# Kernel tuning notes

Hardware: AMD Instinct MI355X
Metric: run time of the kernel (lower is better)

Reference implementation:

```python
import jax, jax.numpy as jnp
import numpy as np

B, S, D, H, FF = 4, 2048, 512, 8, 2048
HD = D // H
SCALE = float(D) ** 0.5  # original scales by sqrt(embed_dim), not sqrt(head_dim)
EPS = 1e-5


def setup_inputs() -> dict:
    key = jax.random.key(0)
    ks = jax.random.split(key, 16)
    s_in = 1.0 / np.sqrt(D)
    s_ff = 1.0 / np.sqrt(FF)
    return {
        "embeddings": jax.random.normal(ks[0], (B, S, D), dtype=jnp.float32),
        "mask": jnp.ones((B, S), dtype=bool),
        # per-head Q/K/V projections stacked: [H, D, HD]
        "Wq": jax.random.uniform(ks[1], (H, D, HD), jnp.float32, -s_in, s_in),
        "bq": jax.random.uniform(ks[2], (H, HD), jnp.float32, -s_in, s_in),
        "Wk": jax.random.uniform(ks[3], (H, D, HD), jnp.float32, -s_in, s_in),
        "bk": jax.random.uniform(ks[4], (H, HD), jnp.float32, -s_in, s_in),
        "Wv": jax.random.uniform(ks[5], (H, D, HD), jnp.float32, -s_in, s_in),
        "bv": jax.random.uniform(ks[6], (H, HD), jnp.float32, -s_in, s_in),
        "Wc": jax.random.uniform(ks[7], (D, D), jnp.float32, -s_in, s_in),
        "bc": jax.random.uniform(ks[8], (D,), jnp.float32, -s_in, s_in),
        "W1": jax.random.uniform(ks[9], (D, FF), jnp.float32, -s_in, s_in),
        "b1": jax.random.uniform(ks[10], (FF,), jnp.float32, -s_in, s_in),
        "W2": jax.random.uniform(ks[11], (FF, D), jnp.float32, -s_ff, s_ff),
        "b2": jax.random.uniform(ks[12], (D,), jnp.float32, -s_ff, s_ff),
        "gamma": jnp.ones((D,), jnp.float32),
        "beta": jnp.zeros((D,), jnp.float32),
    }


def reference(embeddings, mask, Wq, bq, Wk, bk, Wv, bv, Wc, bc, W1, b1, W2, b2, gamma, beta):
    # Per-head projections batched into one einsum each: [B,H,S,HD]
    Q = jnp.einsum("bsd,hdf->bhsf", embeddings, Wq) + bq[:, None, :]
    K = jnp.einsum("bsd,hdf->bhsf", embeddings, Wk) + bk[:, None, :]
    V = jnp.einsum("bsd,hdf->bhsf", embeddings, Wv) + bv[:, None, :]
    # NOTE: the original computes a masked score tensor but then softmaxes the
    # UNMASKED scores (bug). We faithfully ignore the mask here.
    scores = jnp.einsum("bhsf,bhtf->bhst", Q, K) / SCALE  # [B,H,S,S]
    A = jax.nn.softmax(scores, axis=-1)
    Hh = jnp.einsum("bhst,bhtf->bhsf", A, V)  # [B,H,S,HD]
    # concat heads along feature dim (head h -> contiguous slice)
    Hcat = jnp.transpose(Hh, (0, 2, 1, 3)).reshape(B, S, D)
    Hp = Hcat @ Wc + bc
    # add & norm (dropout is identity at eval)
    res = Hp + embeddings
    mu = jnp.mean(res, axis=-1, keepdims=True)
    var = jnp.var(res, axis=-1, keepdims=True)
    Hn = (res - mu) / jnp.sqrt(var + EPS) * gamma + beta
    out = jax.nn.relu(Hn @ W1 + b1) @ W2 + b2  # no residual after FFN in original
    return out, mask
```

## Files before the change

kernel.cpp:

```cpp
#include <hip/hip_runtime.h>
#include <hip/hip_bf16.h>
#include <cstdint>
#include <cstddef>

typedef short  s16x8 __attribute__((ext_vector_type(8)));
typedef short  s16x4 __attribute__((ext_vector_type(4)));
typedef float  f32x4 __attribute__((ext_vector_type(4)));
typedef unsigned u32x2 __attribute__((ext_vector_type(2)));

static constexpr int Bb = 4, Ss = 2048, Dd = 512, Hh = 8, HDd = 64, FFf = 2048;
static constexpr int Mm = Bb * Ss;

__device__ __forceinline__ unsigned short f2bf(float f) {
  unsigned u = __float_as_uint(f);
  u += 0x7FFFu + ((u >> 16) & 1u);
  return (unsigned short)(u >> 16);
}

__device__ __forceinline__ unsigned cvt_pk_bf16(float lo, float hi) {
  unsigned r;
  asm("v_cvt_pk_bf16_f32 %0, %1, %2" : "=v"(r) : "v"(lo), "v"(hi));
  return r;
}

#define GLOAD_LDS16(gp, lp)                                                     \
  __builtin_amdgcn_global_load_lds((const __attribute__((address_space(1))) void*)(gp), \
                                   (__attribute__((address_space(3))) void*)(lp), 16, 0, 0)

__device__ __forceinline__ void xpose_tile(const float* __restrict__ in,
                                           unsigned short* __restrict__ out,
                                           int K, int N, int bx, int by, float (*t)[33]) {
  const int lx = threadIdx.x & 31, ly = threadIdx.x >> 5;
  const int n0 = bx * 32, k0 = by * 32;
#pragma unroll
  for (int r = 0; r < 4; ++r) t[ly + r * 8][lx] = in[(size_t)(k0 + ly + r * 8) * N + n0 + lx];
  __syncthreads();
#pragma unroll
  for (int r = 0; r < 4; ++r)
    out[(size_t)(n0 + ly + r * 8) * K + k0 + lx] = f2bf(t[lx][ly + r * 8]);
}

__global__ __launch_bounds__(256) void prep_all(
    const float* __restrict__ emb, const float* __restrict__ Wq, const float* __restrict__ Wk,
    const float* __restrict__ Wv, const float* __restrict__ Wc, const float* __restrict__ W1,
    const float* __restrict__ W2, unsigned short* __restrict__ embB,
    unsigned short* __restrict__ WtQKV, unsigned short* __restrict__ WtC,
    unsigned short* __restrict__ Wt1, unsigned short* __restrict__ Wt2,
    float* __restrict__ maskOut) {
  __shared__ float t[32][33];
  const int blk = blockIdx.x;
  if (blk < 4096) {
    const int i = blk * 256 + threadIdx.x;
    const float4 v = reinterpret_cast<const float4*>(emb)[i];
    s16x4 o; o[0] = f2bf(v.x); o[1] = f2bf(v.y); o[2] = f2bf(v.z); o[3] = f2bf(v.w);
    reinterpret_cast<s16x4*>(embB)[i] = o;
  } else if (blk < 4864) {
    const int b = blk - 4096;
    const int bx = b & 15, by = (b >> 4) & 1, z = b >> 5;
    const int sel = z >> 3, h = z & 7;
    const float* W = sel == 0 ? Wq : (sel == 1 ? Wk : Wv);
    const float* inb = W + (size_t)h * 512 * 64;
    unsigned short* outb = WtQKV + (size_t)sel * 512 * 512 + (size_t)h * 64 * 512;
    const int lx = threadIdx.x & 31, ly = threadIdx.x >> 5;
    const int d0 = bx * 32, f0 = by * 32;
#pragma unroll
    for (int r = 0; r < 4; ++r) t[ly + r * 8][lx] = inb[(size_t)(d0 + ly + r * 8) * 64 + f0 + lx];
    __syncthreads();
#pragma unroll
    for (int r = 0; r < 4; ++r)
      outb[(size_t)(f0 + ly + r * 8) * 512 + d0 + lx] = f2bf(t[lx][ly + r * 8]);
  } else if (blk < 5120) {
    const int b = blk - 4864;
    xpose_tile(Wc, WtC, 512, 512, b & 15, b >> 4, t);
  } else if (blk < 6144) {
    const int b = blk - 5120;
    xpose_tile(W1, Wt1, 512, 2048, b & 63, b >> 6, t);
  } else if (blk < 7168) {
    const int b = blk - 6144;
    xpose_tile(W2, Wt2, 2048, 512, b & 15, b >> 4, t);
  } else {
    const int i = (blk - 7168) * 256 + threadIdx.x;
    if (i < Bb * Ss) maskOut[i] = 1.0f;
  }
}

template<int EPI, int NI>
__global__ __launch_bounds__(256) void gemm_bt(
    const unsigned short* __restrict__ A, const unsigned short* __restrict__ Bt,
    const float* __restrict__ bias0, const float* __restrict__ bias1, const float* __restrict__ bias2,
    const float* __restrict__ addf, float* __restrict__ outF,
    unsigned short* __restrict__ outB0, unsigned short* __restrict__ outB1,
    unsigned short* __restrict__ outB2, int M, int N, int K) {
  constexpr int BN = NI * 32;
  __shared__ alignas(16) unsigned short As[3][128 * 32];
  __shared__ alignas(16) unsigned short Bs[3][BN * 32];
  const int tid = threadIdx.x;
  const int lane = tid & 63, wid = tid >> 6;
  const int wr = wid >> 1, wc = wid & 1;
  const int fr = lane & 15, kg = lane >> 4;
  const int m0 = blockIdx.y * 128, n0 = blockIdx.x * BN;

  const unsigned short* gA = A + (size_t)(m0 + (tid >> 2)) * K + ((tid & 3) << 3);
  const unsigned short* gB = Bt + (size_t)(n0 + ((tid >> 2) & (BN - 1))) * K + ((tid & 3) << 3);

  auto STAGE = [&](int kt, int buf) {
    unsigned short* lA = &As[buf][wid * 512];
    unsigned short* lB = &Bs[buf][wid * 512];
    GLOAD_LDS16(gA + kt, lA);
    GLOAD_LDS16(gA + (size_t)64 * K + kt, lA + 2048);
    GLOAD_LDS16(gB + kt, lB);
    if constexpr (NI == 4) GLOAD_LDS16(gB + (size_t)64 * K + kt, lB + 2048);
  };

  f32x4 acc[4][NI];
#pragma unroll
  for (int i = 0; i < 4; ++i)
#pragma unroll
    for (int j = 0; j < NI; ++j)
#pragma unroll
      for (int r = 0; r < 4; ++r) acc[i][j][r] = 0.f;

  STAGE(0, 0);
  STAGE(32, 1);
  const int nk = K >> 5;
  int cur = 0;
  for (int ki = 0; ki < nk; ++ki) {
    const int pre = cur == 0 ? 2 : cur - 1;
    __builtin_amdgcn_s_barrier();
    if (ki + 2 < nk) {
      STAGE((ki + 2) << 5, pre);
      if constexpr (NI == 4)
        asm volatile("s_waitcnt vmcnt(8)" ::: "memory");
      else
        asm volatile("s_waitcnt vmcnt(6)" ::: "memory");
    } else if (ki + 1 < nk) {
      if constexpr (NI == 4)
        asm volatile("s_waitcnt vmcnt(4)" ::: "memory");
      else
        asm volatile("s_waitcnt vmcnt(3)" ::: "memory");
    } else {
      asm volatile("s_waitcnt vmcnt(0)" ::: "memory");
    }
    __builtin_amdgcn_sched_barrier(0);
    __builtin_amdgcn_s_barrier();
    __builtin_amdgcn_sched_barrier(0);

    s16x8 af[4], bfv[NI];
#pragma unroll
    for (int i = 0; i < 4; ++i)
      af[i] = *reinterpret_cast<const s16x8*>(&As[cur][(wr * 64 + i * 16 + fr) * 32 + kg * 8]);
#pragma unroll
    for (int i = 0; i < NI; ++i)
      bfv[i] = *reinterpret_cast<const s16x8*>(
          &Bs[cur][(wc * (NI * 16) + i * 16 + fr) * 32 + kg * 8]);
#pragma unroll
    for (int mi = 0; mi < 4; ++mi)
#pragma unroll
      for (int ni = 0; ni < NI; ++ni)
        acc[mi][ni] = __builtin_amdgcn_mfma_f32_16x16x32_bf16(af[mi], bfv[ni], acc[mi][ni], 0, 0, 0);
    cur = cur == 2 ? 0 : cur + 1;
  }

#pragma unroll
  for (int mi = 0; mi < 4; ++mi)
#pragma unroll
    for (int ni = 0; ni < NI; ++ni)
#pragma unroll
      for (int r = 0; r < 4; ++r) {
        const int row = m0 + wr * 64 + mi * 16 + kg * 4 + r;
        const int col = n0 + wc * (NI * 16) + ni * 16 + fr;
        float v = acc[mi][ni][r];
        if constexpr (EPI == 0) {
          const int sel = col >> 9, c = col & 511;
          const float* bs = sel == 0 ? bias0 : (sel == 1 ? bias1 : bias2);
          v += bs[c];
          const int b = row >> 11, s = row & 2047;
          const int h = c >> 6, f = c & 63;
          if (sel == 0)
            outB0[((size_t)((b << 3) + h) * 2048 + s) * 64 + f] = f2bf(v);
          else if (sel == 1)
            outB1[((size_t)((b << 3) + h) * 2048 + s) * 64 + f] = f2bf(v);
          else
            outB2[((size_t)((b << 3) + h) * 64 + f) * 2048 + s] = f2bf(v);
        } else if constexpr (EPI == 1) {
          const size_t idx = (size_t)row * 512 + col;
          outF[idx] = v + bias0[col] + addf[idx];
        } else if constexpr (EPI == 2) {
          v += bias0[col];
          outB0[(size_t)row * 2048 + col] = f2bf(v > 0.f ? v : 0.f);
        } else {
          outF[(size_t)row * 512 + col] = v + bias0[col];
        }
      }
}

__global__ __launch_bounds__(256) void attn_kernel(const unsigned short* __restrict__ Q,
                                                   const unsigned short* __restrict__ Kx,
                                                   const unsigned short* __restrict__ V,
                                                   unsigned short* __restrict__ Hcat) {
  const int lane = threadIdx.x & 63, wid = threadIdx.x >> 6;
  const int fr = lane & 15, kg = lane >> 4;
  const int lin = blockIdx.x;
  const int xcd = lin & 7, idx = lin >> 3;
  const int bh = xcd * 4 + (idx & 3);
  const int qi = idx >> 2;
  const int b = bh >> 3, h = bh & 7;
  const int q0 = qi * 64 + wid * 16;
  const unsigned short* Qh = Q + (size_t)bh * Ss * HDd;
  const unsigned short* Kh = Kx + (size_t)bh * Ss * HDd;
  const unsigned short* Vh = V + (size_t)bh * HDd * Ss;

  __shared__ alignas(16) unsigned short Ks[2][64 * 64];
  __shared__ alignas(16) unsigned short Vs[64 * 64];
  __shared__ alignas(16) unsigned short P[4][16][72];

  const int srow = lane >> 3;
  const int scol = ((lane & 7) ^ srow) << 3;
  const unsigned short* gK0 = Kh + (size_t)(8 * (2 * wid + 0) + srow) * 64 + scol;
  const unsigned short* gK1 = Kh + (size_t)(8 * (2 * wid + 1) + srow) * 64 + scol;
  const unsigned short* gV0 = Vh + (size_t)(8 * (2 * wid + 0) + srow) * 2048 + scol;
  const unsigned short* gV1 = Vh + (size_t)(8 * (2 * wid + 1) + srow) * 2048 + scol;
  unsigned short* lK0a = &Ks[0][(2 * wid + 0) * 512];
  unsigned short* lK1a = &Ks[0][(2 * wid + 1) * 512];
  unsigned short* lK0b = &Ks[1][(2 * wid + 0) * 512];
  unsigned short* lK1b = &Ks[1][(2 * wid + 1) * 512];
  unsigned short* lV0 = &Vs[(2 * wid + 0) * 512];
  unsigned short* lV1 = &Vs[(2 * wid + 1) * 512];

  s16x8 bq[2];
#pragma unroll
  for (int kb = 0; kb < 2; ++kb)
    bq[kb] = *reinterpret_cast<const s16x8*>(&Qh[(size_t)(q0 + fr) * 64 + kb * 32 + kg * 8]);

  f32x4 o[4];
#pragma unroll
  for (int ct = 0; ct < 4; ++ct)
#pragma unroll
    for (int r = 0; r < 4; ++r) o[ct][r] = 0.f;
  float mr = -1e30f, lsum = 0.f;

  const float iscL = 1.4426950408889634f * 0.044194173824159216f;
  const int swz = (fr & 7) << 3;

  GLOAD_LDS16(gK0, lK0a);
  GLOAD_LDS16(gK1, lK1a);
  GLOAD_LDS16(gV0, lV0);
  GLOAD_LDS16(gV1, lV1);

#pragma unroll 1
  for (int t = 0; t < 32; ++t) {
    const int kt = t * 64;
    const int ktn = (kt + 64) & 2047;
    const unsigned short* KsC = Ks[t & 1];
    unsigned short* nK0 = (t & 1) ? lK0a : lK0b;
    unsigned short* nK1 = (t & 1) ? lK1a : lK1b;

    asm volatile("s_waitcnt vmcnt(2)" ::: "memory");
    __builtin_amdgcn_sched_barrier(0);
    __builtin_amdgcn_s_barrier();
    __builtin_amdgcn_sched_barrier(0);

    f32x4 sc[4];
#pragma unroll
    for (int ct = 0; ct < 4; ++ct)
#pragma unroll
      for (int r = 0; r < 4; ++r) sc[ct][r] = 0.f;
#pragma unroll
    for (int ct = 0; ct < 4; ++ct)
#pragma unroll
      for (int kb = 0; kb < 2; ++kb) {
        const s16x8 kf = *reinterpret_cast<const s16x8*>(
            &KsC[(ct * 16 + fr) * 64 + (((kg << 3) + (kb << 5)) ^ swz)]);
        sc[ct] = __builtin_amdgcn_mfma_f32_16x16x32_bf16(kf, bq[kb], sc[ct], 0, 0, 0);
      }

    GLOAD_LDS16(gK0 + (size_t)ktn * 64, nK0);
    GLOAD_LDS16(gK1 + (size_t)ktn * 64, nK1);

    float mxl;
    {
      const float a0 = fmaxf(fmaxf(sc[0][0], sc[0][1]), fmaxf(sc[0][2], sc[0][3]));
      const float a1 = fmaxf(fmaxf(sc[1][0], sc[1][1]), fmaxf(sc[1][2], sc[1][3]));
      const float a2 = fmaxf(fmaxf(sc[2][0], sc[2][1]), fmaxf(sc[2][2], sc[2][3]));
      const float a3 = fmaxf(fmaxf(sc[3][0], sc[3][1]), fmaxf(sc[3][2], sc[3][3]));
      mxl = fmaxf(fmaxf(a0, a1), fmaxf(a2, a3)) * iscL;
    }
    if (!__all(mxl <= mr + 8.0f)) {
      float mx = fmaxf(mxl, __shfl_xor(mxl, 16));
      mx = fmaxf(mx, __shfl_xor(mx, 32));
      const float mn = fmaxf(mr, mx);
      const float corr = exp2f(mr - mn);
      mr = mn;
      lsum *= corr;
      float corrq[4];
#pragma unroll
      for (int r = 0; r < 4; ++r) corrq[r] = __shfl(corr, kg * 4 + r);
#pragma unroll
      for (int ct = 0; ct < 4; ++ct)
#pragma unroll
        for (int r = 0; r < 4; ++r) o[ct][r] *= corrq[r];
    }

    float ps0 = 0.f, ps1 = 0.f;
#pragma unroll
    for (int ct = 0; ct < 4; ++ct) {
      float p0 = exp2f(__builtin_fmaf(sc[ct][0], iscL, -mr));
      float p1 = exp2f(__builtin_fmaf(sc[ct][1], iscL, -mr));
      float p2 = exp2f(__builtin_fmaf(sc[ct][2], iscL, -mr));
      float p3 = exp2f(__builtin_fmaf(sc[ct][3], iscL, -mr));
      ps0 += (p0 + p1);
      ps1 += (p2 + p3);
      u32x2 pk;
      pk[0] = cvt_pk_bf16(p0, p1);
      pk[1] = cvt_pk_bf16(p2, p3);
      *reinterpret_cast<u32x2*>(&P[wid][fr][ct * 16 + kg * 4]) = pk;
    }
    lsum += ps0 + ps1;

    asm volatile("s_waitcnt vmcnt(2)" ::: "memory");
    __builtin_amdgcn_sched_barrier(0);
    __builtin_amdgcn_s_barrier();
    __builtin_amdgcn_sched_barrier(0);

    const s16x8 pa0 = *reinterpret_cast<const s16x8*>(&P[wid][fr][kg * 8]);
    const s16x8 pa1 = *reinterpret_cast<const s16x8*>(&P[wid][fr][32 + kg * 8]);
#pragma unroll
    for (int ct = 0; ct < 4; ++ct) {
      const s16x8 bv0 = *reinterpret_cast<const s16x8*>(
          &Vs[(ct * 16 + fr) * 64 + (((kg << 3) + 0) ^ swz)]);
      o[ct] = __builtin_amdgcn_mfma_f32_16x16x32_bf16(pa0, bv0, o[ct], 0, 0, 0);
      const s16x8 bv1 = *reinterpret_cast<const s16x8*>(
          &Vs[(ct * 16 + fr) * 64 + (((kg << 3) + 32) ^ swz)]);
      o[ct] = __builtin_amdgcn_mfma_f32_16x16x32_bf16(pa1, bv1, o[ct], 0, 0, 0);
    }

    __builtin_amdgcn_s_barrier();
    __builtin_amdgcn_sched_barrier(0);
    GLOAD_LDS16(gV0 + ktn, lV0);
    GLOAD_LDS16(gV1 + ktn, lV1);
  }

  lsum += __shfl_xor(lsum, 16);
  lsum += __shfl_xor(lsum, 32);
  float invq[4];
#pragma unroll
  for (int r = 0; r < 4; ++r) invq[r] = 1.0f / __shfl(lsum, kg * 4 + r);
#pragma unroll
  for (int ct = 0; ct < 4; ++ct)
#pragma unroll
    for (int r = 0; r < 4; ++r) {
      const int qrow = q0 + kg * 4 + r;
      Hcat[(size_t)(b * Ss + qrow) * Dd + h * 64 + ct * 16 + fr] = f2bf(o[ct][r] * invq[r]);
    }
}

__global__ __launch_bounds__(256) void layernorm_k(const float* __restrict__ res,
                                                   const float* __restrict__ gamma,
                                                   const float* __restrict__ beta,
                                                   unsigned short* __restrict__ out) {
  const int lane = threadIdx.x & 63, wid = threadIdx.x >> 6;
  const int row = blockIdx.x * 4 + wid;
  const float* rp = res + (size_t)row * 512 + lane * 8;
  const float4 v0 = *reinterpret_cast<const float4*>(rp);
  const float4 v1 = *reinterpret_cast<const float4*>(rp + 4);
  float x[8] = {v0.x, v0.y, v0.z, v0.w, v1.x, v1.y, v1.z, v1.w};
  float s = 0.f, q = 0.f;
#pragma unroll
  for (int j = 0; j < 8; ++j) { s += x[j]; q += x[j] * x[j]; }
#pragma unroll
  for (int off = 32; off; off >>= 1) { s += __shfl_xor(s, off); q += __shfl_xor(q, off); }
  const float mean = s * (1.f / 512.f);
  const float var = q * (1.f / 512.f) - mean * mean;
  const float rstd = rsqrtf(var + 1e-5f);
  s16x8 o;
#pragma unroll
  for (int j = 0; j < 8; ++j) {
    const int c = lane * 8 + j;
    o[j] = f2bf((x[j] - mean) * rstd * gamma[c] + beta[c]);
  }
  *reinterpret_cast<s16x8*>(out + (size_t)row * 512 + lane * 8) = o;
}

extern "C" void kernel_launch(void* const* d_in, const int* in_sizes, int n_in,
                              void* d_out, int out_size, void* d_ws, size_t ws_size,
                              hipStream_t stream) {
  const float* emb = (const float*)d_in[0];
  const float* Wq = (const float*)d_in[2];
  const float* bq = (const float*)d_in[3];
  const float* Wk = (const float*)d_in[4];
  const float* bk = (const float*)d_in[5];
  const float* Wv = (const float*)d_in[6];
  const float* bv = (const float*)d_in[7];
  const float* Wc = (const float*)d_in[8];
  const float* bc = (const float*)d_in[9];
  const float* W1 = (const float*)d_in[10];
  const float* b1 = (const float*)d_in[11];
  const float* W2 = (const float*)d_in[12];
  const float* b2 = (const float*)d_in[13];
  const float* gamma = (const float*)d_in[14];
  const float* beta = (const float*)d_in[15];
  float* out = (float*)d_out;

  char* ws = (char*)d_ws;
  size_t off = 0;
  auto alloc = [&](size_t bytes) {
    char* p = ws + off;
    off = (off + bytes + 255) & ~(size_t)255;
    return p;
  };
  unsigned short* embB = (unsigned short*)alloc((size_t)Mm * Dd * 2);
  unsigned short* WtQKV = (unsigned short*)alloc((size_t)1536 * 512 * 2);
  unsigned short* WtC = (unsigned short*)alloc((size_t)512 * 512 * 2);
  unsigned short* Wt1 = (unsigned short*)alloc((size_t)2048 * 512 * 2);
  unsigned short* Wt2 = (unsigned short*)alloc((size_t)512 * 2048 * 2);
  unsigned short* Qb = (unsigned short*)alloc((size_t)Mm * Dd * 2);
  unsigned short* Kb = (unsigned short*)alloc((size_t)Mm * Dd * 2);
  unsigned short* Vt = (unsigned short*)alloc((size_t)Mm * Dd * 2);
  unsigned short* Hcat = (unsigned short*)alloc((size_t)Mm * Dd * 2);
  float* resF = (float*)alloc((size_t)Mm * Dd * 4);
  unsigned short* HnB = (unsigned short*)alloc((size_t)Mm * Dd * 2);
  unsigned short* G = Qb;

  prep_all<<<7200, 256, 0, stream>>>(emb, Wq, Wk, Wv, Wc, W1, W2,
                                     embB, WtQKV, WtC, Wt1, Wt2,
                                     out + (size_t)Mm * Dd);

  gemm_bt<0, 4><<<dim3(12, 64), 256, 0, stream>>>(embB, WtQKV, bq, bk, bv, nullptr, nullptr,
                                                  Qb, Kb, Vt, Mm, 1536, 512);
  attn_kernel<<<1024, 256, 0, stream>>>(Qb, Kb, Vt, Hcat);
  gemm_bt<1, 2><<<dim3(8, 64), 256, 0, stream>>>(Hcat, WtC, bc, nullptr, nullptr, emb, resF,
                                                 nullptr, nullptr, nullptr, Mm, 512, 512);
  layernorm_k<<<2048, 256, 0, stream>>>(resF, gamma, beta, HnB);
  gemm_bt<2, 4><<<dim3(16, 64), 256, 0, stream>>>(HnB, Wt1, b1, nullptr, nullptr, nullptr, nullptr,
                                                  G, nullptr, nullptr, Mm, 2048, 512);
  gemm_bt<3, 2><<<dim3(8, 64), 256, 0, stream>>>(G, Wt2, b2, nullptr, nullptr, nullptr, out,
                                                 nullptr, nullptr, nullptr, Mm, 512, 2048);
}
```

Baseline: 202.1 us.

## Load V tiles directly into registers instead of staging through LDS

The attention kernel drops the shared-memory V staging buffer. Each lane now loads its V MFMA operands straight from global memory into registers, prefetching the next tile after the PV MMAs. This removes two block barriers per iteration and the LDS reads for V, and the K prefetch is issued earlier, right after the first barrier. In exchange every wave loads the full V tile redundantly from global or L2 memory, register pressure rises, and the vmcnt wait counts become trickier to keep correct.

After: 268.0 us. 1.33x slower.

```diff
diff --git a/kernel.cpp b/kernel.cpp
--- a/kernel.cpp
+++ b/kernel.cpp
@@ -211,21 +211,18 @@
   const unsigned short* Vh = V + (size_t)bh * HDd * Ss;
 
   __shared__ alignas(16) unsigned short Ks[2][64 * 64];
-  __shared__ alignas(16) unsigned short Vs[64 * 64];
   __shared__ alignas(16) unsigned short P[4][16][72];
 
   const int srow = lane >> 3;
   const int scol = ((lane & 7) ^ srow) << 3;
   const unsigned short* gK0 = Kh + (size_t)(8 * (2 * wid + 0) + srow) * 64 + scol;
   const unsigned short* gK1 = Kh + (size_t)(8 * (2 * wid + 1) + srow) * 64 + scol;
-  const unsigned short* gV0 = Vh + (size_t)(8 * (2 * wid + 0) + srow) * 2048 + scol;
-  const unsigned short* gV1 = Vh + (size_t)(8 * (2 * wid + 1) + srow) * 2048 + scol;
   unsigned short* lK0a = &Ks[0][(2 * wid + 0) * 512];
   unsigned short* lK1a = &Ks[0][(2 * wid + 1) * 512];
   unsigned short* lK0b = &Ks[1][(2 * wid + 0) * 512];
   unsigned short* lK1b = &Ks[1][(2 * wid + 1) * 512];
-  unsigned short* lV0 = &Vs[(2 * wid + 0) * 512];
-  unsigned short* lV1 = &Vs[(2 * wid + 1) * 512];
+
+  const unsigned short* Vp = Vh + (size_t)fr * Ss + kg * 8;
 
   s16x8 bq[2];
 #pragma unroll
@@ -244,21 +241,28 @@
 
   GLOAD_LDS16(gK0, lK0a);
   GLOAD_LDS16(gK1, lK1a);
-  GLOAD_LDS16(gV0, lV0);
-  GLOAD_LDS16(gV1, lV1);
+  s16x8 vreg[8];
+#pragma unroll
+  for (int ct = 0; ct < 4; ++ct)
+#pragma unroll
+    for (int kb = 0; kb < 2; ++kb)
+      vreg[ct * 2 + kb] = *reinterpret_cast<const s16x8*>(
+          &Vp[(size_t)(ct * 16) * Ss + kb * 32]);
 
 #pragma unroll 1
   for (int t = 0; t < 32; ++t) {
-    const int kt = t * 64;
-    const int ktn = (kt + 64) & 2047;
+    const int ktn = (t * 64 + 64) & 2047;
     const unsigned short* KsC = Ks[t & 1];
     unsigned short* nK0 = (t & 1) ? lK0a : lK0b;
     unsigned short* nK1 = (t & 1) ? lK1a : lK1b;
 
-    asm volatile("s_waitcnt vmcnt(2)" ::: "memory");
+    asm volatile("s_waitcnt vmcnt(8)" ::: "memory");
     __builtin_amdgcn_sched_barrier(0);
     __builtin_amdgcn_s_barrier();
     __builtin_amdgcn_sched_barrier(0);
+
+    GLOAD_LDS16(gK0 + (size_t)ktn * 64, nK0);
+    GLOAD_LDS16(gK1 + (size_t)ktn * 64, nK1);
 
     f32x4 sc[4];
 #pragma unroll
@@ -273,9 +277,6 @@
             &KsC[(ct * 16 + fr) * 64 + (((kg << 3) + (kb << 5)) ^ swz)]);
         sc[ct] = __builtin_amdgcn_mfma_f32_16x16x32_bf16(kf, bq[kb], sc[ct], 0, 0, 0);
       }
-
-    GLOAD_LDS16(gK0 + (size_t)ktn * 64, nK0);
-    GLOAD_LDS16(gK1 + (size_t)ktn * 64, nK1);
 
     float mxl;
     {
@@ -319,25 +320,22 @@
 
     asm volatile("s_waitcnt vmcnt(2)" ::: "memory");
     __builtin_amdgcn_sched_barrier(0);
-    __builtin_amdgcn_s_barrier();
-    __builtin_amdgcn_sched_barrier(0);
 
     const s16x8 pa0 = *reinterpret_cast<const s16x8*>(&P[wid][fr][kg * 8]);
     const s16x8 pa1 = *reinterpret_cast<const s16x8*>(&P[wid][fr][32 + kg * 8]);
 #pragma unroll
     for (int ct = 0; ct < 4; ++ct) {
-      const s16x8 bv0 = *reinterpret_cast<const s16x8*>(
-          &Vs[(ct * 16 + fr) * 64 + (((kg << 3) + 0) ^ swz)]);
-      o[ct] = __builtin_amdgcn_mfma_f32_16x16x32_bf16(pa0, bv0, o[ct], 0, 0, 0);
-      const s16x8 bv1 = *reinterpret_cast<const s16x8*>(
-          &Vs[(ct * 16 + fr) * 64 + (((kg << 3) + 32) ^ swz)]);
-      o[ct] = __builtin_amdgcn_mfma_f32_16x16x32_bf16(pa1, bv1, o[ct], 0, 0, 0);
-    }
-
-    __builtin_amdgcn_s_barrier();
-    __builtin_amdgcn_sched_barrier(0);
-    GLOAD_LDS16(gV0 + ktn, lV0);
-    GLOAD_LDS16(gV1 + ktn, lV1);
+      o[ct] = __builtin_amdgcn_mfma_f32_16x16x32_bf16(pa0, vreg[ct * 2 + 0], o[ct], 0, 0, 0);
+      o[ct] = __builtin_amdgcn_mfma_f32_16x16x32_bf16(pa1, vreg[ct * 2 + 1], o[ct], 0, 0, 0);
+    }
+
+    __builtin_amdgcn_sched_barrier(0);
+#pragma unroll
+    for (int ct = 0; ct < 4; ++ct)
+#pragma unroll
+      for (int kb = 0; kb < 2; ++kb)
+        vreg[ct * 2 + kb] = *reinterpret_cast<const s16x8*>(
+            &Vp[(size_t)(ct * 16) * Ss + ktn + kb * 32]);
   }
 
   lsum += __shfl_xor(lsum, 16);
```
